# Optimization experiments

Measured on AMD Instinct MI355X. Metric: run time of the kernel, lower is better.

## Reference

```python
import jax, jax.numpy as jnp
import numpy as np

EMBED_DIM = 1024
NUM_HEADS = 16
D_K = EMBED_DIM // NUM_HEADS
B, T = 4, 2048


def setup_inputs() -> dict:
    key = jax.random.key(0)
    k_x, k_wqkv, k_wo = jax.random.split(key, 3)
    x = jax.random.normal(k_x, (B, T, EMBED_DIM), dtype=jnp.float32)
    # kaiming_normal on torch Linear weight [out,in]: std = sqrt(2/fan_in)=sqrt(2/embed_dim)
    std = np.sqrt(2.0 / EMBED_DIM).astype(np.float32)
    # store weights already transposed to [in, out] for y = x @ W + b
    W_qkv = jax.random.normal(k_wqkv, (EMBED_DIM, 3 * EMBED_DIM), dtype=jnp.float32) * std
    b_qkv = jnp.zeros((3 * EMBED_DIM,), dtype=jnp.float32)
    W_o = jax.random.normal(k_wo, (EMBED_DIM, EMBED_DIM), dtype=jnp.float32) * std
    b_o = jnp.zeros((EMBED_DIM,), dtype=jnp.float32)
    return {"x": x, "W_qkv": W_qkv, "b_qkv": b_qkv, "W_o": W_o, "b_o": b_o}


def reference(x, W_qkv, b_qkv, W_o, b_o):
    Bsz, Tlen, D = x.shape
    qkv = x @ W_qkv + b_qkv                      # [B,T,3D]
    q, k, v = jnp.split(qkv, 3, axis=-1)
    # split heads -> [B,H,T,d_k]
    def heads(t):
        return t.reshape(Bsz, Tlen, NUM_HEADS, D_K).transpose(0, 2, 1, 3)
    q, k, v = heads(q), heads(k), heads(v)
    scores = jnp.einsum('bhqd,bhkd->bhqk', q, k) / jnp.sqrt(jnp.float32(D_K))
    causal = jnp.tril(jnp.ones((Tlen, Tlen), dtype=bool))
    scores = jnp.where(causal[None, None], scores, -jnp.inf)
    attn = jax.nn.softmax(scores, axis=-1)
    out = jnp.einsum('bhqk,bhkd->bhqd', attn, v)  # [B,H,T,d_k]
    out = out.transpose(0, 2, 1, 3).reshape(Bsz, Tlen, D)
    return out @ W_o + b_o
```

## Files before the change

kernel.cpp:

```cpp
#include <hip/hip_runtime.h>
#include <hip/hip_bf16.h>
#include <math.h>

typedef unsigned short u16;
typedef __attribute__((ext_vector_type(8))) short bf16x8;
typedef __attribute__((ext_vector_type(4))) float f32x4;

#define BATCH 4
#define TSEQ  2048
#define HEADS 16
#define DK    64
#define EMB   1024
#define MROWS 8192
#define NQKV  3072
#define PHT   ((size_t)MROWS * EMB)

__device__ __forceinline__ u16 f2bf(float f) {
    union { float f; unsigned int i; } v;
    v.f = f;
    unsigned int x = v.i;
    return (u16)((x + 0x7FFFu + ((x >> 16) & 1u)) >> 16);
}

__device__ __forceinline__ unsigned int pk2bf(float a, float b) {
    float2 f2; f2.x = a; f2.y = b;
    union { __hip_bfloat162 h; unsigned int u; } cv;
    cv.h = __float22bfloat162_rn(f2);
    return cv.u;
}

__device__ __forceinline__ void gl2lds16(const u16* g, u16* l) {
    __builtin_amdgcn_global_load_lds(
        (const __attribute__((address_space(1))) unsigned int*)g,
        (__attribute__((address_space(3))) unsigned int*)l, 16, 0, 0);
}

__global__ __launch_bounds__(256) void convert_x(const float* __restrict__ X,
                                                 u16* __restrict__ Xb) {
    int i = (blockIdx.x * 256 + threadIdx.x) * 4;
    float4 v = *(const float4*)&X[i];
    ushort4 o;
    o.x = f2bf(v.x); o.y = f2bf(v.y); o.z = f2bf(v.z); o.w = f2bf(v.w);
    *(ushort4*)&Xb[i] = o;
}

__global__ __launch_bounds__(256) void transpose_both(const float* __restrict__ Wqkv,
                                                      const float* __restrict__ Wo,
                                                      u16* __restrict__ Wt,
                                                      u16* __restrict__ Wot) {
    __shared__ float tile[32][33];
    const int tx = threadIdx.x & 31, ty = threadIdx.x >> 5;
    const int K = 1024;
    const float* W;
    u16* D;
    int N, bx;
    if (blockIdx.x < 96) { W = Wqkv; D = Wt; N = 3072; bx = blockIdx.x; }
    else                 { W = Wo;   D = Wot; N = 1024; bx = blockIdx.x - 96; }
    const int by = blockIdx.y;
#pragma unroll
    for (int s = 0; s < 4; s++)
        tile[ty + 8 * s][tx] = W[(size_t)(by * 32 + ty + 8 * s) * N + bx * 32 + tx];
    __syncthreads();
#pragma unroll
    for (int s = 0; s < 4; s++)
        D[(size_t)(bx * 32 + ty + 8 * s) * K + by * 32 + tx] = f2bf(tile[tx][ty + 8 * s]);
}

template <int KDIM>
__device__ __forceinline__ void gemm_core(const u16* __restrict__ A,
                                          const u16* __restrict__ Bt,
                                          u16* As, u16* Bs,
                                          int m0, int n0, int wm, int wn,
                                          int tid, int lo, int quad,
                                          f32x4 (&acc)[4][4]) {
    for (int k0 = 0; k0 < KDIM; k0 += 32) {
        __syncthreads();
#pragma unroll
        for (int c = 0; c < 2; c++) {
            int chunk = c * 256 + tid;
            int row = chunk >> 2, p = chunk & 3;
            int pg = p ^ ((row >> 1) & 3);
            gl2lds16(A + (size_t)(m0 + row) * KDIM + k0 + pg * 8, As + chunk * 8);
            gl2lds16(Bt + (size_t)(n0 + row) * KDIM + k0 + pg * 8, Bs + chunk * 8);
        }
        __syncthreads();
        bf16x8 af[4], bw[4];
#pragma unroll
        for (int i = 0; i < 4; i++) {
            int r = wm + i * 16 + lo;
            int pp = quad ^ ((r >> 1) & 3);
            af[i] = *(const bf16x8*)&As[r * 32 + pp * 8];
        }
#pragma unroll
        for (int j = 0; j < 4; j++) {
            int r = wn + j * 16 + lo;
            int pp = quad ^ ((r >> 1) & 3);
            bw[j] = *(const bf16x8*)&Bs[r * 32 + pp * 8];
        }
#pragma unroll
        for (int i = 0; i < 4; i++)
#pragma unroll
            for (int j = 0; j < 4; j++)
                acc[i][j] = __builtin_amdgcn_mfma_f32_16x16x32_bf16(
                    af[i], bw[j], acc[i][j], 0, 0, 0);
    }
}

__global__ __launch_bounds__(256) void gemm1_mfma(const u16* __restrict__ A,
                                                  const u16* __restrict__ Bt,
                                                  const float* __restrict__ bias,
                                                  u16* __restrict__ qkv) {
    __shared__ u16 As[128 * 32];
    __shared__ u16 Bs[128 * 32];
    const int tid = threadIdx.x;
    const int lane = tid & 63, wv = tid >> 6;
    const int lo = lane & 15, quad = lane >> 4;
    const int m0 = blockIdx.y * 128, n0 = blockIdx.x * 128;
    const int wm = (wv >> 1) * 64, wn = (wv & 1) * 64;
    const float scale2 = 0.18033688011112042f;
    f32x4 acc[4][4] = {};

    gemm_core<1024>(A, Bt, As, Bs, m0, n0, wm, wn, tid, lo, quad, acc);

    const int whichw = (n0 + wn) >> 10;
    if (whichw == 2) {
#pragma unroll
        for (int i = 0; i < 4; i++) {
            int mb = m0 + wm + i * 16 + quad * 4;
            int b = mb >> 11, t = mb & 2047;
#pragma unroll
            for (int j = 0; j < 4; j++) {
                int n = n0 + wn + j * 16 + lo;
                int rem = n & 1023;
                int h = rem >> 6, d = rem & 63;
                float bn = bias[n];
                ushort4 o;
                o.x = f2bf(acc[i][j][0] + bn);
                o.y = f2bf(acc[i][j][1] + bn);
                o.z = f2bf(acc[i][j][2] + bn);
                o.w = f2bf(acc[i][j][3] + bn);
                *(ushort4*)&qkv[2 * PHT +
                                (((size_t)(b * HEADS + h) * DK + d) * TSEQ + t)] = o;
            }
        }
    } else {
        const float sc = (whichw == 0) ? scale2 : 1.0f;
#pragma unroll
        for (int i = 0; i < 4; i++) {
#pragma unroll
            for (int r = 0; r < 4; r++) {
                int m = m0 + wm + i * 16 + quad * 4 + r;
                int b = m >> 11, t = m & 2047;
#pragma unroll
                for (int j = 0; j < 4; j++) {
                    int n = n0 + wn + j * 16 + lo;
                    float v = (acc[i][j][r] + bias[n]) * sc;
                    int rem = n & 1023;
                    int h = rem >> 6, d = rem & 63;
                    qkv[(size_t)whichw * PHT +
                        (((size_t)(b * HEADS + h) * TSEQ + t) * DK + d)] = f2bf(v);
                }
            }
        }
    }
}

__global__ __launch_bounds__(256) void gemm2_mfma(const u16* __restrict__ A,
                                                  const u16* __restrict__ Bt,
                                                  const float* __restrict__ bias,
                                                  float* __restrict__ out) {
    __shared__ u16 As[128 * 32];
    __shared__ u16 Bs[128 * 32];
    const int tid = threadIdx.x;
    const int lane = tid & 63, wv = tid >> 6;
    const int lo = lane & 15, quad = lane >> 4;
    const int m0 = blockIdx.y * 128, n0 = blockIdx.x * 128;
    const int wm = (wv >> 1) * 64, wn = (wv & 1) * 64;
    f32x4 acc[4][4] = {};

    gemm_core<1024>(A, Bt, As, Bs, m0, n0, wm, wn, tid, lo, quad, acc);

#pragma unroll
    for (int i = 0; i < 4; i++) {
#pragma unroll
        for (int r = 0; r < 4; r++) {
            int m = m0 + wm + i * 16 + quad * 4 + r;
#pragma unroll
            for (int j = 0; j < 4; j++) {
                int n = n0 + wn + j * 16 + lo;
                out[(size_t)m * EMB + n] = acc[i][j][r] + bias[n];
            }
        }
    }
}

__global__ __launch_bounds__(256, 2) void attn_mfma(const u16* __restrict__ Qg,
                                                    const u16* __restrict__ Kg,
                                                    const u16* __restrict__ Vg,
                                                    u16* __restrict__ AO) {
    __shared__ u16 pool[5 * 8192];
    u16* Rr = pool + 4 * 8192;

    const int tid = threadIdx.x;
    const int lane = tid & 63, wv = tid >> 6;
    const int lo = lane & 15, quad = lane >> 4;
    const int pair = blockIdx.x, bh = blockIdx.y;
    const size_t base = (size_t)bh * TSEQ * DK;
    const int b = bh >> 4, h = bh & 15;
    const bf16x8 onesf = {0x3F80, 0x3F80, 0x3F80, 0x3F80,
                          0x3F80, 0x3F80, 0x3F80, 0x3F80};

    auto stageKV = [&](int kt2, int bufsel) {
        u16* Kd = pool + bufsel * 8192;
        u16* Vd = pool + 2 * 8192 + bufsel * 8192;
#pragma unroll
        for (int c = 0; c < 4; c++) {
            int chunk = c * 256 + tid;
            int row = chunk >> 3, p = chunk & 7;
            int pg = p ^ (row & 7);
            gl2lds16(Kg + base + (size_t)(kt2 * 128 + row) * DK + pg * 8,
                     Kd + chunk * 8);
        }
#pragma unroll
        for (int c = 0; c < 4; c++) {
            int chunk = c * 256 + tid;
            int row = chunk >> 4, p = chunk & 15;
            int pg = p ^ (row & 15);
            gl2lds16(Vg + base + (size_t)row * TSEQ + kt2 * 128 + pg * 8,
                     Vd + chunk * 8);
        }
    };

    for (int qi = 0; qi < 2; qi++) {
        const int qt = qi ? (15 - pair) : pair;
        const int q0 = qt * 128;

        __syncthreads();
#pragma unroll
        for (int c = 0; c < 4; c++) {
            int chunk = c * 256 + tid;
            int row = chunk >> 3, p = chunk & 7;
            int pg = p ^ (row & 7);
            gl2lds16(Qg + base + (size_t)(q0 + row) * DK + pg * 8, Rr + chunk * 8);
        }
        stageKV(0, 0);
        __syncthreads();

        bf16x8 bq[2][2];
#pragma unroll
        for (int i = 0; i < 2; i++)
#pragma unroll
            for (int hh = 0; hh < 2; hh++) {
                int row = wv * 32 + i * 16 + lo;
                int ch = (hh * 4 + quad) ^ (row & 7);
                bq[i][hh] = *(const bf16x8*)&Rr[row * 64 + ch * 8];
            }

        f32x4 O[2][5] = {};

        for (int kt = 0; kt <= qt; kt++) {
            const int cur = kt & 1;
            if (kt) __syncthreads();
            if (kt < qt) stageKV(kt + 1, cur ^ 1);
            const u16* Ksc = pool + cur * 8192;
            const u16* Vtc = pool + 2 * 8192 + cur * 8192;

            const bool diag = (kt == qt);
            u16* Ps = Rr + wv * 2048;

#pragma unroll
            for (int jh = 0; jh < 2; jh++) {
                f32x4 st[4][2] = {};
#pragma unroll
                for (int hh = 0; hh < 2; hh++) {
#pragma unroll
                    for (int j2 = 0; j2 < 4; j2++) {
                        int row = (jh * 4 + j2) * 16 + lo;
                        int ch = (hh * 4 + quad) ^ (row & 7);
                        bf16x8 ak = *(const bf16x8*)&Ksc[row * 64 + ch * 8];
                        st[j2][0] = __builtin_amdgcn_mfma_f32_16x16x32_bf16(
                            ak, bq[0][hh], st[j2][0], 0, 0, 0);
                        st[j2][1] = __builtin_amdgcn_mfma_f32_16x16x32_bf16(
                            ak, bq[1][hh], st[j2][1], 0, 0, 0);
                    }
                }
#pragma unroll
                for (int j2 = 0; j2 < 4; j2++) {
#pragma unroll
                    for (int i = 0; i < 2; i++) {
                        float e[4];
#pragma unroll
                        for (int r = 0; r < 4; r++)
                            e[r] = __builtin_amdgcn_exp2f(st[j2][i][r]);
                        if (diag) {
                            int qr = q0 + wv * 32 + i * 16 + lo;
                            int kb = kt * 128 + (jh * 4 + j2) * 16 + quad * 4;
#pragma unroll
                            for (int r = 0; r < 4; r++)
                                if (kb + r > qr) e[r] = 0.f;
                        }
                        uint2 w;
                        w.x = pk2bf(e[0], e[1]);
                        w.y = pk2bf(e[2], e[3]);
                        int rowl = i * 16 + lo;
                        int chp = (2 * j2 + (quad >> 1)) ^ (lo & 7);
                        *(uint2*)&Ps[rowl * 64 + chp * 8 + (quad & 1) * 4] = w;
                    }
                }
#pragma unroll
                for (int hp = 0; hp < 2; hp++) {
                    bf16x8 ap[2], bv[4];
#pragma unroll
                    for (int i = 0; i < 2; i++) {
                        int rowl = i * 16 + lo;
                        int ch = (4 * hp + quad) ^ (lo & 7);
                        ap[i] = *(const bf16x8*)&Ps[rowl * 64 + ch * 8];
                    }
#pragma unroll
                    for (int jn = 0; jn < 4; jn++) {
                        int vrow = jn * 16 + lo;
                        int ch = (8 * jh + 4 * hp + quad) ^ (vrow & 15);
                        bv[jn] = *(const bf16x8*)&Vtc[vrow * 128 + ch * 8];
                    }
#pragma unroll
                    for (int i = 0; i < 2; i++) {
#pragma unroll
                        for (int jn = 0; jn < 4; jn++)
                            O[i][jn] = __builtin_amdgcn_mfma_f32_16x16x32_bf16(
                                ap[i], bv[jn], O[i][jn], 0, 0, 0);
                        O[i][4] = __builtin_amdgcn_mfma_f32_16x16x32_bf16(
                            ap[i], onesf, O[i][4], 0, 0, 0);
                    }
                }
            }
        }

#pragma unroll
        for (int i = 0; i < 2; i++)
#pragma unroll
            for (int r = 0; r < 4; r++) {
                int qrow = q0 + wv * 32 + i * 16 + quad * 4 + r;
                float inv = 1.f / O[i][4][r];
#pragma unroll
                for (int jn = 0; jn < 4; jn++) {
                    int d = jn * 16 + lo;
                    AO[(((size_t)b * TSEQ + qrow) * HEADS + h) * DK + d] =
                        f2bf(O[i][jn][r] * inv);
                }
            }
    }
}

extern "C" void kernel_launch(void* const* d_in, const int* in_sizes, int n_in,
                              void* d_out, int out_size, void* d_ws, size_t ws_size,
                              hipStream_t stream) {
    const float* x    = (const float*)d_in[0];
    const float* Wqkv = (const float*)d_in[1];
    const float* bqkv = (const float*)d_in[2];
    const float* Wo   = (const float*)d_in[3];
    const float* bo   = (const float*)d_in[4];
    float* out = (float*)d_out;

    u16* Xb  = (u16*)d_ws;
    u16* Wt  = Xb + PHT;
    u16* Wot = Wt + (size_t)NQKV * EMB;
    u16* qkv = Wot + (size_t)EMB * EMB;
    u16* AO  = Xb;

    convert_x<<<MROWS * EMB / 1024, 256, 0, stream>>>(x, Xb);
    transpose_both<<<dim3(96 + 32, 32), 256, 0, stream>>>(Wqkv, Wo, Wt, Wot);

    gemm1_mfma<<<dim3(NQKV / 128, MROWS / 128), 256, 0, stream>>>(Xb, Wt, bqkv, qkv);
    attn_mfma<<<dim3(8, BATCH * HEADS), 256, 0, stream>>>(
        qkv, qkv + PHT, qkv + 2 * PHT, AO);
    gemm2_mfma<<<dim3(EMB / 128, MROWS / 128), 256, 0, stream>>>(AO, Wot, bo, out);
}
```

Measured before the change: 254.6 us.

## Rewrite GEMM core with 128x256 tiles, triple-buffered async LDS pipeline and grid swizzle

Replaces the single-buffered 128x128, K=32 GEMM mainloop with a 512-thread, 128x256 tile and K=64 steps. Loads run through a three-stage LDS ring using direct global-to-LDS copies, with explicit vmcnt waits and raw barriers so loads overlap MFMA work. It also raises MFMA priority and swizzles block order so neighbouring blocks share tiles in L2. The cost is about 144KB of LDS per block, which allows only one block per CU, and hand-tuned waitcnt counts that must match the number of outstanding loads exactly.

```diff
diff --git a/kernel.cpp b/kernel.cpp
--- a/kernel.cpp
+++ b/kernel.cpp
@@ -67,60 +67,108 @@
 }
 
 template <int KDIM>
-__device__ __forceinline__ void gemm_core(const u16* __restrict__ A,
-                                          const u16* __restrict__ Bt,
-                                          u16* As, u16* Bs,
-                                          int m0, int n0, int wm, int wn,
-                                          int tid, int lo, int quad,
-                                          f32x4 (&acc)[4][4]) {
-    for (int k0 = 0; k0 < KDIM; k0 += 32) {
-        __syncthreads();
+__device__ __forceinline__ void gemm_core256(const u16* __restrict__ A,
+                                             const u16* __restrict__ Bt,
+                                             u16* pool,
+                                             int m0, int n0, int wm, int wn,
+                                             int tid, int lo, int quad,
+                                             f32x4 (&acc)[4][4]) {
+    constexpr int NT = KDIM / 64;
+
+    const u16* ga[2];
+    const u16* gb[4];
+#pragma unroll
+    for (int c = 0; c < 2; c++) {
+        int chunk = c * 512 + tid, row = chunk >> 3, p = chunk & 7;
+        ga[c] = A + (size_t)(m0 + row) * KDIM + (p ^ (row & 7)) * 8;
+    }
+#pragma unroll
+    for (int c = 0; c < 4; c++) {
+        int chunk = c * 512 + tid, row = chunk >> 3, p = chunk & 7;
+        gb[c] = Bt + (size_t)(n0 + row) * KDIM + (p ^ (row & 7)) * 8;
+    }
+
+    auto stage = [&](int b) {
+        u16* As = pool + b * 24576;
+        u16* Bs = As + 8192;
 #pragma unroll
         for (int c = 0; c < 2; c++) {
-            int chunk = c * 256 + tid;
-            int row = chunk >> 2, p = chunk & 3;
-            int pg = p ^ ((row >> 1) & 3);
-            gl2lds16(A + (size_t)(m0 + row) * KDIM + k0 + pg * 8, As + chunk * 8);
-            gl2lds16(Bt + (size_t)(n0 + row) * KDIM + k0 + pg * 8, Bs + chunk * 8);
-        }
-        __syncthreads();
-        bf16x8 af[4], bw[4];
-#pragma unroll
-        for (int i = 0; i < 4; i++) {
-            int r = wm + i * 16 + lo;
-            int pp = quad ^ ((r >> 1) & 3);
-            af[i] = *(const bf16x8*)&As[r * 32 + pp * 8];
-        }
-#pragma unroll
-        for (int j = 0; j < 4; j++) {
-            int r = wn + j * 16 + lo;
-            int pp = quad ^ ((r >> 1) & 3);
-            bw[j] = *(const bf16x8*)&Bs[r * 32 + pp * 8];
-        }
-#pragma unroll
-        for (int i = 0; i < 4; i++)
-#pragma unroll
-            for (int j = 0; j < 4; j++)
-                acc[i][j] = __builtin_amdgcn_mfma_f32_16x16x32_bf16(
-                    af[i], bw[j], acc[i][j], 0, 0, 0);
-    }
-}
-
-__global__ __launch_bounds__(256) void gemm1_mfma(const u16* __restrict__ A,
-                                                  const u16* __restrict__ Bt,
-                                                  const float* __restrict__ bias,
-                                                  u16* __restrict__ qkv) {
-    __shared__ u16 As[128 * 32];
-    __shared__ u16 Bs[128 * 32];
+            gl2lds16(ga[c], As + (size_t)(c * 512 + tid) * 8);
+            ga[c] += 64;
+        }
+#pragma unroll
+        for (int c = 0; c < 4; c++) {
+            gl2lds16(gb[c], Bs + (size_t)(c * 512 + tid) * 8);
+            gb[c] += 64;
+        }
+    };
+
+    auto comp = [&](int b, bool dostage) {
+        const u16* As = pool + b * 24576;
+        const u16* Bs = As + 8192;
+        __builtin_amdgcn_s_barrier();
+        bf16x8 af[2][4], bw[2][4];
+#pragma unroll
+        for (int ks = 0; ks < 2; ks++) {
+#pragma unroll
+            for (int i = 0; i < 4; i++) {
+                int r = wm + i * 16 + lo;
+                af[ks][i] = *(const bf16x8*)&As[r * 64 + ((ks * 4 + quad) ^ (r & 7)) * 8];
+            }
+#pragma unroll
+            for (int j = 0; j < 4; j++) {
+                int r = wn + j * 16 + lo;
+                bw[ks][j] = *(const bf16x8*)&Bs[r * 64 + ((ks * 4 + quad) ^ (r & 7)) * 8];
+            }
+        }
+        asm volatile("s_waitcnt lgkmcnt(0)" ::: "memory");
+        __builtin_amdgcn_s_barrier();
+        if (dostage) stage(b);
+        __builtin_amdgcn_s_setprio(1);
+#pragma unroll
+        for (int ks = 0; ks < 2; ks++)
+#pragma unroll
+            for (int i = 0; i < 4; i++)
+#pragma unroll
+                for (int j = 0; j < 4; j++)
+                    acc[i][j] = __builtin_amdgcn_mfma_f32_16x16x32_bf16(
+                        af[ks][i], bw[ks][j], acc[i][j], 0, 0, 0);
+        __builtin_amdgcn_s_setprio(0);
+    };
+
+    stage(0); stage(1); stage(2);
+    int bsel = 0;
+    for (int kt = 0; kt < NT - 3; kt++) {
+        asm volatile("s_waitcnt vmcnt(12)" ::: "memory");
+        comp(bsel, true);
+        bsel = (bsel == 2) ? 0 : bsel + 1;
+    }
+    asm volatile("s_waitcnt vmcnt(12)" ::: "memory");
+    comp(bsel, false); bsel = (bsel == 2) ? 0 : bsel + 1;
+    asm volatile("s_waitcnt vmcnt(6)" ::: "memory");
+    comp(bsel, false); bsel = (bsel == 2) ? 0 : bsel + 1;
+    asm volatile("s_waitcnt vmcnt(0)" ::: "memory");
+    comp(bsel, false);
+}
+
+__global__ __launch_bounds__(512, 1) void gemm1_mfma(const u16* __restrict__ A,
+                                                     const u16* __restrict__ Bt,
+                                                     const float* __restrict__ bias,
+                                                     u16* __restrict__ qkv) {
+    __shared__ u16 pool[3 * 24576];
     const int tid = threadIdx.x;
     const int lane = tid & 63, wv = tid >> 6;
     const int lo = lane & 15, quad = lane >> 4;
-    const int m0 = blockIdx.y * 128, n0 = blockIdx.x * 128;
-    const int wm = (wv >> 1) * 64, wn = (wv & 1) * 64;
+    const int gx = 12;
+    int lin = blockIdx.y * gx + blockIdx.x;
+    int swz = (lin & 7) * 96 + (lin >> 3);
+    const int n0 = (swz % gx) * 256;
+    const int m0 = (swz / gx) * 128;
+    const int wm = (wv >> 2) * 64, wn = (wv & 3) * 64;
     const float scale2 = 0.18033688011112042f;
     f32x4 acc[4][4] = {};
 
-    gemm_core<1024>(A, Bt, As, Bs, m0, n0, wm, wn, tid, lo, quad, acc);
+    gemm_core256<1024>(A, Bt, pool, m0, n0, wm, wn, tid, lo, quad, acc);
 
     const int whichw = (n0 + wn) >> 10;
     if (whichw == 2) {
@@ -165,20 +213,22 @@
     }
 }
 
-__global__ __launch_bounds__(256) void gemm2_mfma(const u16* __restrict__ A,
-                                                  const u16* __restrict__ Bt,
-                                                  const float* __restrict__ bias,
-                                                  float* __restrict__ out) {
-    __shared__ u16 As[128 * 32];
-    __shared__ u16 Bs[128 * 32];
+__global__ __launch_bounds__(512, 1) void gemm2_mfma(const u16* __restrict__ A,
+                                                     const u16* __restrict__ Bt,
+                                                     const float* __restrict__ bias,
+                                                     float* __restrict__ out) {
+    __shared__ u16 pool[3 * 24576];
     const int tid = threadIdx.x;
     const int lane = tid & 63, wv = tid >> 6;
     const int lo = lane & 15, quad = lane >> 4;
-    const int m0 = blockIdx.y * 128, n0 = blockIdx.x * 128;
-    const int wm = (wv >> 1) * 64, wn = (wv & 1) * 64;
+    int lin = blockIdx.y * 4 + blockIdx.x;
+    int swz = (lin & 7) * 32 + (lin >> 3);
+    const int n0 = (swz & 3) * 256;
+    const int m0 = (swz >> 2) * 128;
+    const int wm = (wv >> 2) * 64, wn = (wv & 3) * 64;
     f32x4 acc[4][4] = {};
 
-    gemm_core<1024>(A, Bt, As, Bs, m0, n0, wm, wn, tid, lo, quad, acc);
+    gemm_core256<1024>(A, Bt, pool, m0, n0, wm, wn, tid, lo, quad, acc);
 
 #pragma unroll
     for (int i = 0; i < 4; i++) {
@@ -370,8 +420,8 @@
     convert_x<<<MROWS * EMB / 1024, 256, 0, stream>>>(x, Xb);
     transpose_both<<<dim3(96 + 32, 32), 256, 0, stream>>>(Wqkv, Wo, Wt, Wot);
 
-    gemm1_mfma<<<dim3(NQKV / 128, MROWS / 128), 256, 0, stream>>>(Xb, Wt, bqkv, qkv);
+    gemm1_mfma<<<dim3(NQKV / 256, MROWS / 128), 512, 0, stream>>>(Xb, Wt, bqkv, qkv);
     attn_mfma<<<dim3(8, BATCH * HEADS), 256, 0, stream>>>(
         qkv, qkv + PHT, qkv + 2 * PHT, AO);
-    gemm2_mfma<<<dim3(EMB / 128, MROWS / 128), 256, 0, stream>>>(AO, Wot, bo, out);
-}
+    gemm2_mfma<<<dim3(EMB / 256, MROWS / 128), 512, 0, stream>>>(AO, Wot, bo, out);
+}
```

Measured after the change: 238.5 us. 1.07x faster.
